# Optimization experiments

Hardware: AMD Instinct MI355X
Metric: run time of the kernel (lower is better)

Reference implementation:

```python
import jax, jax.numpy as jnp
import numpy as np

B, L, D = 4, 4096, 1024
NEG_BIG = -1e30  # finite stand-in for log(0) to keep vjp NaN-free; exp underflows to 0


def log_g(x):
    # log of g(x) = where(x>=0, x+0.5, sigmoid(x)); log-space, branch-safe
    return jnp.where(x >= 0.0, jnp.log(jax.nn.relu(x) + 0.5), -jax.nn.softplus(-x))


def setup_inputs() -> dict:
    key = jax.random.key(0)
    ks = jax.random.split(key, 4)
    std = np.sqrt(2.0 / D)  # kaiming_normal for fan_in = D
    x = jax.random.normal(ks[0], (B, L, D), dtype=jnp.float32)
    W_f = jax.random.normal(ks[1], (D, D), dtype=jnp.float32) * std
    W_i = jax.random.normal(ks[2], (D, D), dtype=jnp.float32) * std
    W_h = jax.random.normal(ks[3], (D, D), dtype=jnp.float32) * std
    b_f = jnp.zeros((D,), dtype=jnp.float32)
    b_i = jnp.zeros((D,), dtype=jnp.float32)
    b_h = jnp.zeros((D,), dtype=jnp.float32)
    return {"x": x, "W_f": W_f, "b_f": b_f, "W_i": W_i, "b_i": b_i, "W_h": W_h, "b_h": b_h}


def reference(x, W_f, b_f, W_i, b_i, W_h, b_h):
    # gate pre-activations: (B, L, D)
    f_pre = jnp.einsum('bld,ed->ble', x, W_f) + b_f
    i_pre = jnp.einsum('bld,ed->ble', x, W_i) + b_i
    h_pre = jnp.einsum('bld,ed->ble', x, W_h) + b_h

    # log-space normalized gates: log_f + log_i parametrize f/(f+i), i/(f+i)
    diff = jax.nn.softplus(-f_pre) - jax.nn.softplus(-i_pre)
    log_f = -jax.nn.softplus(diff)
    log_i = -jax.nn.softplus(-diff)
    log_tilde_h = log_g(h_pre)

    b, l, d = x.shape
    log_h0 = jnp.full((b, 1, d), NEG_BIG, dtype=x.dtype)  # log(0)
    log_values = jnp.concatenate([log_h0, log_i + log_tilde_h], axis=1)  # (B, L+1, D)

    # associative parallel scan in log space
    a_star = jnp.pad(jnp.cumsum(log_f, axis=1), ((0, 0), (1, 0), (0, 0)))  # (B, L+1, D)
    log_h = a_star + jax.lax.cumlogsumexp(log_values - a_star, axis=1)
    return jnp.exp(log_h)[:, 1:]  # (B, L, D)
```

## Files before the change

kernel.cpp:

```cpp
#include <hip/hip_runtime.h>

#define M_TOTAL 16384
#define N_DIM   1024
#define K_DIM   1024
#define L_SEQ   4096
#define B_SZ    4
#define D_DIM   1024
#define CH      64
#define NCHUNK  (L_SEQ / CH)
#define NCHAN   (B_SZ * D_DIM)

#define BM 128
#define BN 128
#define BK 64
#define NKT (K_DIM / BK)
#define TPB 512

typedef __attribute__((ext_vector_type(8))) short v8s;
typedef __attribute__((ext_vector_type(4))) float f32x4;

#define SB0()   __builtin_amdgcn_sched_barrier(0)
#define BAR()   __builtin_amdgcn_s_barrier()
#define WAITL0() do { asm volatile("s_waitcnt lgkmcnt(0)" ::: "memory"); SB0(); } while (0)
#define WAITV6() do { asm volatile("s_waitcnt vmcnt(6)"   ::: "memory"); SB0(); } while (0)
#define WAITV4() do { asm volatile("s_waitcnt vmcnt(4)"   ::: "memory"); SB0(); } while (0)
#define WAITV0() do { asm volatile("s_waitcnt vmcnt(0)"   ::: "memory"); SB0(); } while (0)
#define AS1 __attribute__((address_space(1)))
#define AS3 __attribute__((address_space(3)))

__device__ __forceinline__ ushort f2b(float f) {
  uint u = __float_as_uint(f);
  u += 0x7FFFu + ((u >> 16) & 1u);
  return (ushort)(u >> 16);
}
__device__ __forceinline__ float b2f(ushort u) {
  return __uint_as_float(((uint)u) << 16);
}

__global__ void cast_f32_bf16(const float* __restrict__ src, ushort* __restrict__ dst, int n4) {
  int i = blockIdx.x * blockDim.x + threadIdx.x;
  if (i >= n4) return;
  float4 v = reinterpret_cast<const float4*>(src)[i];
  ushort4 o = make_ushort4(f2b(v.x), f2b(v.y), f2b(v.z), f2b(v.w));
  reinterpret_cast<ushort4*>(dst)[i] = o;
}

__device__ __forceinline__ void gates(float fp, float ip, float hp, float& a, float& v) {
  float Ef = __expf(-fp);
  float Ei = __expf(-ip);
  float r  = __builtin_amdgcn_rcpf(2.f + Ef + Ei);
  float f  = (1.f + Ei) * r;
  float i  = (1.f + Ef) * r;
  float ht = (hp >= 0.f) ? (hp + 0.5f) : __builtin_amdgcn_rcpf(1.f + __expf(-hp));
  a = f;
  v = i * ht;
}

__launch_bounds__(TPB, 2)
__global__ void gemm_fused(const ushort* __restrict__ X,
                           const ushort* __restrict__ W0, const ushort* __restrict__ W1,
                           const ushort* __restrict__ W2,
                           const float* __restrict__ bfp, const float* __restrict__ bip,
                           const float* __restrict__ bhp,
                           uint* __restrict__ Pav)
{
  __shared__ ushort lds[2][4][BM * BK];

  const int id = blockIdx.x;
  const int sw = (id & 7) * 128 + (id >> 3);
  const int n0 = (sw & 7) * BN;
  const int m0 = (sw >> 3) * BM;

  const int tid  = threadIdx.x;
  const int lane = tid & 63;
  const int w    = tid >> 6;
  const int wr   = w >> 2;
  const int wc   = w & 3;
  const int fr   = lane & 15, g = lane >> 4;

  int aoffh[4][2], boffh[2][2];
#pragma unroll
  for (int q = 0; q < 4; ++q)
#pragma unroll
    for (int ks = 0; ks < 2; ++ks) {
      int row = wr * 64 + q * 16 + fr;
      aoffh[q][ks] = row * BK + (((ks * 4 + g) ^ (row & 7)) << 3);
    }
#pragma unroll
  for (int n = 0; n < 2; ++n)
#pragma unroll
    for (int ks = 0; ks < 2; ++ks) {
      int row = wc * 32 + n * 16 + fr;
      boffh[n][ks] = row * BK + (((ks * 4 + g) ^ (row & 7)) << 3);
    }

  const int s0 = tid, s1 = 512 + tid;
  const int r0 = s0 >> 3, k0 = (s0 & 7) ^ (r0 & 7);
  const int r1 = s1 >> 3, k1 = (s1 & 7) ^ (r1 & 7);
  const int d0 = s0 * 8, d1 = s1 * 8;

  const ushort* gsrc[4][2];
  gsrc[0][0] = X  + (size_t)(m0 + r0) * K_DIM + k0 * 8;
  gsrc[0][1] = X  + (size_t)(m0 + r1) * K_DIM + k1 * 8;
  gsrc[1][0] = W0 + (size_t)(n0 + r0) * K_DIM + k0 * 8;
  gsrc[1][1] = W0 + (size_t)(n0 + r1) * K_DIM + k1 * 8;
  gsrc[2][0] = W1 + (size_t)(n0 + r0) * K_DIM + k0 * 8;
  gsrc[2][1] = W1 + (size_t)(n0 + r1) * K_DIM + k1 * 8;
  gsrc[3][0] = W2 + (size_t)(n0 + r0) * K_DIM + k0 * 8;
  gsrc[3][1] = W2 + (size_t)(n0 + r1) * K_DIM + k1 * 8;

  auto issue = [&](int buf, int mat, int kt, int j) {
    const ushort* s_ = gsrc[mat][j] + kt * BK;
    __builtin_amdgcn_global_load_lds((const AS1 void*)s_,
        (AS3 void*)(&lds[buf][mat][j ? d1 : d0]), 16, 0, 0);
  };

  f32x4 acc[3][4][2] = {};

#pragma unroll
  for (int mat = 0; mat < 4; ++mat) { issue(0, mat, 0, 0); issue(0, mat, 0, 1); }
  WAITV4();
  BAR(); SB0();

  int cur = 0;
  for (int t = 0; t < NKT; ++t) {
    const bool pf = (t + 1 < NKT);
    const ushort* rb = &lds[cur][0][0];
    v8s aF[4][2], bF[2][2];

#pragma unroll
    for (int q = 0; q < 4; ++q)
#pragma unroll
      for (int ks = 0; ks < 2; ++ks)
        aF[q][ks] = *reinterpret_cast<const v8s*>(rb + aoffh[q][ks]);
#pragma unroll
    for (int n = 0; n < 2; ++n)
#pragma unroll
      for (int ks = 0; ks < 2; ++ks)
        bF[n][ks] = *reinterpret_cast<const v8s*>(rb + 1 * BM * BK + boffh[n][ks]);
    if (pf) { issue(cur ^ 1, 0, t + 1, 0); issue(cur ^ 1, 0, t + 1, 1);
              issue(cur ^ 1, 1, t + 1, 0); issue(cur ^ 1, 1, t + 1, 1); }
    SB0(); WAITL0();
    __builtin_amdgcn_s_setprio(1);
#pragma unroll
    for (int ks = 0; ks < 2; ++ks)
#pragma unroll
      for (int mi = 0; mi < 4; ++mi) {
        acc[0][mi][0] = __builtin_amdgcn_mfma_f32_16x16x32_bf16(aF[mi][ks], bF[0][ks], acc[0][mi][0], 0, 0, 0);
        acc[0][mi][1] = __builtin_amdgcn_mfma_f32_16x16x32_bf16(aF[mi][ks], bF[1][ks], acc[0][mi][1], 0, 0, 0);
      }
    __builtin_amdgcn_s_setprio(0);
    WAITV6(); BAR(); SB0();

#pragma unroll
    for (int n = 0; n < 2; ++n)
#pragma unroll
      for (int ks = 0; ks < 2; ++ks)
        bF[n][ks] = *reinterpret_cast<const v8s*>(rb + 2 * BM * BK + boffh[n][ks]);
    if (pf) { issue(cur ^ 1, 2, t + 1, 0); issue(cur ^ 1, 2, t + 1, 1); }
    SB0(); WAITL0();
    __builtin_amdgcn_s_setprio(1);
#pragma unroll
    for (int ks = 0; ks < 2; ++ks)
#pragma unroll
      for (int mi = 0; mi < 4; ++mi) {
        acc[1][mi][0] = __builtin_amdgcn_mfma_f32_16x16x32_bf16(aF[mi][ks], bF[0][ks], acc[1][mi][0], 0, 0, 0);
        acc[1][mi][1] = __builtin_amdgcn_mfma_f32_16x16x32_bf16(aF[mi][ks], bF[1][ks], acc[1][mi][1], 0, 0, 0);
      }
    __builtin_amdgcn_s_setprio(0);
    WAITV6(); BAR(); SB0();

#pragma unroll
    for (int n = 0; n < 2; ++n)
#pragma unroll
      for (int ks = 0; ks < 2; ++ks)
        bF[n][ks] = *reinterpret_cast<const v8s*>(rb + 3 * BM * BK + boffh[n][ks]);
    if (pf) { issue(cur ^ 1, 3, t + 1, 0); issue(cur ^ 1, 3, t + 1, 1); }
    SB0(); WAITL0();
    __builtin_amdgcn_s_setprio(1);
#pragma unroll
    for (int ks = 0; ks < 2; ++ks)
#pragma unroll
      for (int mi = 0; mi < 4; ++mi) {
        acc[2][mi][0] = __builtin_amdgcn_mfma_f32_16x16x32_bf16(aF[mi][ks], bF[0][ks], acc[2][mi][0], 0, 0, 0);
        acc[2][mi][1] = __builtin_amdgcn_mfma_f32_16x16x32_bf16(aF[mi][ks], bF[1][ks], acc[2][mi][1], 0, 0, 0);
      }
    __builtin_amdgcn_s_setprio(0);

    if (pf) {
      if (t + 2 == NKT) { WAITV0(); } else { WAITV4(); }
      BAR(); SB0();
      cur ^= 1;
    }
  }

#pragma unroll
  for (int ni = 0; ni < 2; ++ni) {
    const int col = n0 + wc * 32 + ni * 16 + fr;
    const float vbf = bfp[col], vbi = bip[col], vbh = bhp[col];
#pragma unroll
    for (int mi = 0; mi < 4; ++mi) {
      const int row0 = m0 + wr * 64 + mi * 16 + g * 4;
#pragma unroll
      for (int r = 0; r < 4; ++r) {
        float a, v;
        gates(acc[0][mi][ni][r] + vbf, acc[1][mi][ni][r] + vbi, acc[2][mi][ni][r] + vbh, a, v);
        Pav[(size_t)(row0 + r) * N_DIM + col] = (uint)f2b(a) | ((uint)f2b(v) << 16);
      }
    }
  }
}

__global__ void scan_pass1(const uint* __restrict__ Pav,
                           float* __restrict__ AggA, float* __restrict__ AggV)
{
  int tid = blockIdx.x * blockDim.x + threadIdx.x;
  int c = tid & (NCHAN - 1);
  int chunk = tid >> 12;
  int d = c & (D_DIM - 1);
  int b = c >> 10;
  size_t base = ((size_t)b * L_SEQ + (size_t)chunk * CH) * D_DIM + d;
  float A = 1.f, V = 0.f;
#pragma unroll 4
  for (int t = 0; t < CH; ++t) {
    uint u = Pav[base + (size_t)t * D_DIM];
    float a = b2f((ushort)(u & 0xFFFFu));
    float v = b2f((ushort)(u >> 16));
    A *= a;
    V = fmaf(a, V, v);
  }
  AggA[chunk * NCHAN + c] = A;
  AggV[chunk * NCHAN + c] = V;
}

__global__ void scan_mid(const float* __restrict__ AggA, const float* __restrict__ AggV,
                         float* __restrict__ Start)
{
  int c = blockIdx.x * blockDim.x + threadIdx.x;
  float h = 0.f;
#pragma unroll
  for (int j = 0; j < NCHUNK; ++j) {
    Start[j * NCHAN + c] = h;
    h = fmaf(AggA[j * NCHAN + c], h, AggV[j * NCHAN + c]);
  }
}

__global__ void scan_pass2(const uint* __restrict__ Pav,
                           const float* __restrict__ Start, float* __restrict__ out)
{
  int tid = blockIdx.x * blockDim.x + threadIdx.x;
  int c = tid & (NCHAN - 1);
  int chunk = tid >> 12;
  int d = c & (D_DIM - 1);
  int b = c >> 10;
  size_t base = ((size_t)b * L_SEQ + (size_t)chunk * CH) * D_DIM + d;
  float h = Start[chunk * NCHAN + c];
#pragma unroll 4
  for (int t = 0; t < CH; ++t) {
    size_t idx = base + (size_t)t * D_DIM;
    uint u = Pav[idx];
    float a = b2f((ushort)(u & 0xFFFFu));
    float v = b2f((ushort)(u >> 16));
    h = fmaf(a, h, v);
    out[idx] = h;
  }
}

extern "C" void kernel_launch(void* const* d_in, const int* in_sizes, int n_in,
                              void* d_out, int out_size, void* d_ws, size_t ws_size,
                              hipStream_t stream) {
  (void)in_sizes; (void)n_in; (void)out_size; (void)ws_size;
  const float* x  = (const float*)d_in[0];
  const float* Wf = (const float*)d_in[1];
  const float* bf = (const float*)d_in[2];
  const float* Wi = (const float*)d_in[3];
  const float* bi = (const float*)d_in[4];
  const float* Wh = (const float*)d_in[5];
  const float* bh = (const float*)d_in[6];
  float* out = (float*)d_out;

  ushort* xb  = (ushort*)d_ws;
  ushort* wfb = xb  + (size_t)M_TOTAL * K_DIM;
  ushort* wib = wfb + (size_t)N_DIM * K_DIM;
  ushort* whb = wib + (size_t)N_DIM * K_DIM;
  uint*  Pav  = (uint*)(whb + (size_t)N_DIM * K_DIM);
  float* AggA  = (float*)(Pav + (size_t)M_TOTAL * N_DIM);
  float* AggV  = AggA + NCHAN * NCHUNK;
  float* Start = AggV + NCHAN * NCHUNK;

  cast_f32_bf16<<<(M_TOTAL * K_DIM / 4) / 256, 256, 0, stream>>>(x,  xb,  M_TOTAL * K_DIM / 4);
  cast_f32_bf16<<<(N_DIM  * K_DIM / 4) / 256, 256, 0, stream>>>(Wf, wfb, N_DIM * K_DIM / 4);
  cast_f32_bf16<<<(N_DIM  * K_DIM / 4) / 256, 256, 0, stream>>>(Wi, wib, N_DIM * K_DIM / 4);
  cast_f32_bf16<<<(N_DIM  * K_DIM / 4) / 256, 256, 0, stream>>>(Wh, whb, N_DIM * K_DIM / 4);

  gemm_fused<<<dim3((M_TOTAL / BM) * (N_DIM / BN)), TPB, 0, stream>>>(
      xb, wfb, wib, whb, bf, bi, bh, Pav);

  scan_pass1<<<(NCHAN * NCHUNK) / 256, 256, 0, stream>>>(Pav, AggA, AggV);
  scan_mid<<<NCHAN / 256, 256, 0, stream>>>(AggA, AggV, Start);
  scan_pass2<<<(NCHAN * NCHUNK) / 256, 256, 0, stream>>>(Pav, Start, out);
}
```

Before: 188.8 us.

## Issue all next-tile loads at once and cut barriers to one per k-step

The fused three-gate GEMM main loop now prefetches all four matrices for the next k-tile in one batch. It uses a single vmcnt(0) wait and barrier per k-step instead of three staggered waits and barriers. B-fragment reads are double-buffered in registers (bA/bB), and lgkmcnt(4) partial waits let MFMAs on one matrix overlap the LDS reads for the next. The aim is to reduce barrier stalls and expose more LDS-read/MFMA overlap. The cost is a full wait on global loads at the end of each step, which can expose more load latency, plus some extra register pressure.

New measurement: 189.8 us. Within noise of the previous version (+0.6%).

```diff
diff --git a/kernel.cpp b/kernel.cpp
--- a/kernel.cpp
+++ b/kernel.cpp
@@ -22,8 +22,7 @@
 #define SB0()   __builtin_amdgcn_sched_barrier(0)
 #define BAR()   __builtin_amdgcn_s_barrier()
 #define WAITL0() do { asm volatile("s_waitcnt lgkmcnt(0)" ::: "memory"); SB0(); } while (0)
-#define WAITV6() do { asm volatile("s_waitcnt vmcnt(6)"   ::: "memory"); SB0(); } while (0)
-#define WAITV4() do { asm volatile("s_waitcnt vmcnt(4)"   ::: "memory"); SB0(); } while (0)
+#define WAITL4() do { asm volatile("s_waitcnt lgkmcnt(4)" ::: "memory"); SB0(); } while (0)
 #define WAITV0() do { asm volatile("s_waitcnt vmcnt(0)"   ::: "memory"); SB0(); } while (0)
 #define AS1 __attribute__((address_space(1)))
 #define AS3 __attribute__((address_space(3)))
@@ -119,14 +118,14 @@
 
 #pragma unroll
   for (int mat = 0; mat < 4; ++mat) { issue(0, mat, 0, 0); issue(0, mat, 0, 1); }
-  WAITV4();
+  WAITV0();
   BAR(); SB0();
 
   int cur = 0;
   for (int t = 0; t < NKT; ++t) {
     const bool pf = (t + 1 < NKT);
     const ushort* rb = &lds[cur][0][0];
-    v8s aF[4][2], bF[2][2];
+    v8s aF[4][2], bA[2][2], bB[2][2];
 
 #pragma unroll
     for (int q = 0; q < 4; ++q)
@@ -137,58 +136,58 @@
     for (int n = 0; n < 2; ++n)
 #pragma unroll
       for (int ks = 0; ks < 2; ++ks)
-        bF[n][ks] = *reinterpret_cast<const v8s*>(rb + 1 * BM * BK + boffh[n][ks]);
-    if (pf) { issue(cur ^ 1, 0, t + 1, 0); issue(cur ^ 1, 0, t + 1, 1);
-              issue(cur ^ 1, 1, t + 1, 0); issue(cur ^ 1, 1, t + 1, 1); }
-    SB0(); WAITL0();
+        bA[n][ks] = *reinterpret_cast<const v8s*>(rb + 1 * BM * BK + boffh[n][ks]);
+    SB0();
+    if (pf) {
+#pragma unroll
+      for (int mat = 0; mat < 4; ++mat) { issue(cur ^ 1, mat, t + 1, 0); issue(cur ^ 1, mat, t + 1, 1); }
+    }
+    SB0();
+#pragma unroll
+    for (int n = 0; n < 2; ++n)
+#pragma unroll
+      for (int ks = 0; ks < 2; ++ks)
+        bB[n][ks] = *reinterpret_cast<const v8s*>(rb + 2 * BM * BK + boffh[n][ks]);
+    SB0();
+    WAITL4();
     __builtin_amdgcn_s_setprio(1);
 #pragma unroll
     for (int ks = 0; ks < 2; ++ks)
 #pragma unroll
       for (int mi = 0; mi < 4; ++mi) {
-        acc[0][mi][0] = __builtin_amdgcn_mfma_f32_16x16x32_bf16(aF[mi][ks], bF[0][ks], acc[0][mi][0], 0, 0, 0);
-        acc[0][mi][1] = __builtin_amdgcn_mfma_f32_16x16x32_bf16(aF[mi][ks], bF[1][ks], acc[0][mi][1], 0, 0, 0);
+        acc[0][mi][0] = __builtin_amdgcn_mfma_f32_16x16x32_bf16(aF[mi][ks], bA[0][ks], acc[0][mi][0], 0, 0, 0);
+        acc[0][mi][1] = __builtin_amdgcn_mfma_f32_16x16x32_bf16(aF[mi][ks], bA[1][ks], acc[0][mi][1], 0, 0, 0);
       }
     __builtin_amdgcn_s_setprio(0);
-    WAITV6(); BAR(); SB0();
-
 #pragma unroll
     for (int n = 0; n < 2; ++n)
 #pragma unroll
       for (int ks = 0; ks < 2; ++ks)
-        bF[n][ks] = *reinterpret_cast<const v8s*>(rb + 2 * BM * BK + boffh[n][ks]);
-    if (pf) { issue(cur ^ 1, 2, t + 1, 0); issue(cur ^ 1, 2, t + 1, 1); }
-    SB0(); WAITL0();
+        bA[n][ks] = *reinterpret_cast<const v8s*>(rb + 3 * BM * BK + boffh[n][ks]);
+    SB0();
+    WAITL4();
     __builtin_amdgcn_s_setprio(1);
 #pragma unroll
     for (int ks = 0; ks < 2; ++ks)
 #pragma unroll
       for (int mi = 0; mi < 4; ++mi) {
-        acc[1][mi][0] = __builtin_amdgcn_mfma_f32_16x16x32_bf16(aF[mi][ks], bF[0][ks], acc[1][mi][0], 0, 0, 0);
-        acc[1][mi][1] = __builtin_amdgcn_mfma_f32_16x16x32_bf16(aF[mi][ks], bF[1][ks], acc[1][mi][1], 0, 0, 0);
+        acc[1][mi][0] = __builtin_amdgcn_mfma_f32_16x16x32_bf16(aF[mi][ks], bB[0][ks], acc[1][mi][0], 0, 0, 0);
+        acc[1][mi][1] = __builtin_amdgcn_mfma_f32_16x16x32_bf16(aF[mi][ks], bB[1][ks], acc[1][mi][1], 0, 0, 0);
       }
     __builtin_amdgcn_s_setprio(0);
-    WAITV6(); BAR(); SB0();
-
-#pragma unroll
-    for (int n = 0; n < 2; ++n)
-#pragma unroll
-      for (int ks = 0; ks < 2; ++ks)
-        bF[n][ks] = *reinterpret_cast<const v8s*>(rb + 3 * BM * BK + boffh[n][ks]);
-    if (pf) { issue(cur ^ 1, 3, t + 1, 0); issue(cur ^ 1, 3, t + 1, 1); }
-    SB0(); WAITL0();
+    WAITL0();
     __builtin_amdgcn_s_setprio(1);
 #pragma unroll
     for (int ks = 0; ks < 2; ++ks)
 #pragma unroll
       for (int mi = 0; mi < 4; ++mi) {
-        acc[2][mi][0] = __builtin_amdgcn_mfma_f32_16x16x32_bf16(aF[mi][ks], bF[0][ks], acc[2][mi][0], 0, 0, 0);
-        acc[2][mi][1] = __builtin_amdgcn_mfma_f32_16x16x32_bf16(aF[mi][ks], bF[1][ks], acc[2][mi][1], 0, 0, 0);
+        acc[2][mi][0] = __builtin_amdgcn_mfma_f32_16x16x32_bf16(aF[mi][ks], bA[0][ks], acc[2][mi][0], 0, 0, 0);
+        acc[2][mi][1] = __builtin_amdgcn_mfma_f32_16x16x32_bf16(aF[mi][ks], bA[1][ks], acc[2][mi][1], 0, 0, 0);
       }
     __builtin_amdgcn_s_setprio(0);
 
     if (pf) {
-      if (t + 2 == NKT) { WAITV0(); } else { WAITV4(); }
+      WAITV0();
       BAR(); SB0();
       cur ^= 1;
     }
```
